# Kernel optimization log

Hardware: AMD Instinct MI355X
Metric: run time of the kernel (lower is better)

## Reference

```python
import jax, jax.numpy as jnp
import numpy as np

TOL = 5               # proximity_tolerance
PROX_REWARD = 2.0     # proximity_reward
FAR_PENALTY = 1.5     # far_penalty
CLASS_WEIGHTS = np.array([0.1, 5.0, 5.0], dtype=np.float32)


def setup_inputs() -> dict:
    key = jax.random.key(0)
    k1, k2 = jax.random.split(key)
    B, S, C = 512, 16384, 3
    logits = jax.random.normal(k1, (B, S, C), dtype=jnp.float32)
    labels = jax.random.randint(k2, (B, S), 0, 3)
    return {"logits": logits, "labels": labels}


def _window_any(mask_bool, tol):
    # True at position p iff mask is True anywhere in [p-tol, p+tol] (clipped at edges).
    pooled = jax.lax.reduce_window(
        mask_bool.astype(jnp.float32), 0.0, jax.lax.max,
        window_dimensions=(1, 2 * tol + 1), window_strides=(1, 1),
        padding=[(0, 0), (tol, tol)])
    return pooled > 0.5


def reference(logits, labels):
    B, S, C = logits.shape
    w = jnp.asarray(CLASS_WEIGHTS)

    valid = labels != -100                      # [B,S]
    labels_safe = jnp.where(valid, labels, 0)

    # Weighted cross-entropy, reduction='none' (weight applied per-element, ignore_index -> 0)
    logp = jax.nn.log_softmax(logits, axis=-1)  # [B,S,C]
    picked = jnp.take_along_axis(logp, labels_safe[..., None], axis=-1)[..., 0]
    base_loss = jnp.where(valid, -w[labels_safe] * picked, 0.0)  # [B,S]

    predictions = jnp.argmax(logits, axis=-1)   # [B,S] int
    pred_sw = predictions >= 1                  # predicted switch positions
    true_sw = labels >= 1                       # true switch positions (-100 < 1 so excluded)

    pred_near = _window_any(pred_sw, TOL)       # any predicted switch within +/-TOL
    true_near = _window_any(true_sw, TOL)       # any true switch within +/-TOL
    has_true = jnp.any(true_sw, axis=1, keepdims=True)  # far-penalty only applies if batch row has true switches

    reward_mask = (true_sw & pred_near).astype(jnp.float32)
    penalty_mask = (pred_sw & (~true_near) & has_true).astype(jnp.float32)
    additive = -PROX_REWARD * reward_mask + FAR_PENALTY * penalty_mask

    vm = valid.astype(jnp.float32)
    return ((base_loss + additive) * vm).sum() / vm.sum()
```

## Files before the change

### kernel.cpp

```cpp
#include <hip/hip_runtime.h>
#include <hip/hip_bf16.h>


#define TOL 5
#define BLOCK 256
#define CHUNK 1024

typedef unsigned long long u64;

__global__ __launch_bounds__(BLOCK) void k1_stream(
    const float* __restrict__ logits, const int* __restrict__ labels,
    u64* __restrict__ pmask, u64* __restrict__ tmask, u64* __restrict__ vmask,
    double* __restrict__ pbsum, int* __restrict__ pvcnt)
{
    __shared__ float lds_l[CHUNK * 3];
    __shared__ int   lds_lab[CHUNK];
    __shared__ float wb[BLOCK / 64];
    __shared__ int   wv[BLOCK / 64];

    const int tid = threadIdx.x;
    const long long chunk = blockIdx.x;

    const float4* gl4 = (const float4*)logits + chunk * (CHUNK * 3 / 4);
    float4* ll4 = (float4*)lds_l;
#pragma unroll
    for (int k = 0; k < 3; ++k) ll4[tid + k * BLOCK] = gl4[tid + k * BLOCK];
    const int4* gi4 = (const int4*)labels + chunk * (CHUNK / 4);
    ((int4*)lds_lab)[tid] = gi4[tid];
    __syncthreads();

    float bsum = 0.f;
    int   vcnt = 0;
    const int wave = tid >> 6;
    const u64 base_group = (u64)chunk * (CHUNK / 64);

#pragma unroll
    for (int q = 0; q < CHUNK / BLOCK; ++q) {
        const int pos = q * BLOCK + tid;
        const float l0 = lds_l[3 * pos + 0];
        const float l1 = lds_l[3 * pos + 1];
        const float l2 = lds_l[3 * pos + 2];
        const int lab = lds_lab[pos];

        const bool valid = (lab != -100);
        const int ls = valid ? lab : 0;

        const float mx = fmaxf(l0, fmaxf(l1, l2));
        const float se = __expf(l0 - mx) + __expf(l1 - mx) + __expf(l2 - mx);
        const float lse = mx + __logf(se);
        const float lpick = (ls == 0 ? l0 : (ls == 1 ? l1 : l2)) - lse;
        const float w = (ls == 0) ? 0.1f : 5.0f;
        bsum += valid ? (-w * lpick) : 0.f;
        vcnt += valid ? 1 : 0;

        const bool psw = fmaxf(l1, l2) > l0;
        const bool tsw = (lab >= 1);

        const u64 pm = __ballot(psw);
        const u64 tm = __ballot(tsw);
        const u64 vm = __ballot(valid);
        if ((tid & 63) == 0) {
            const u64 g = base_group + (u64)(q * (BLOCK / 64) + wave);
            pmask[g] = pm; tmask[g] = tm; vmask[g] = vm;
        }
    }

#pragma unroll
    for (int off = 32; off; off >>= 1) {
        bsum += __shfl_down(bsum, off);
        vcnt += __shfl_down(vcnt, off);
    }
    if ((tid & 63) == 0) { wb[wave] = bsum; wv[wave] = vcnt; }
    __syncthreads();
    if (tid == 0) {
        double s = 0.0; int c = 0;
#pragma unroll
        for (int i = 0; i < BLOCK / 64; ++i) { s += (double)wb[i]; c += wv[i]; }
        pbsum[chunk] = s;
        pvcnt[chunk] = c;
    }
}

__global__ __launch_bounds__(BLOCK) void k2_window(
    const u64* __restrict__ pmask, const u64* __restrict__ tmask,
    const u64* __restrict__ vmask, float* __restrict__ adj_row)
{
    const int row = blockIdx.x;
    const int t = threadIdx.x;
    const int GPR = BLOCK;
    const long long base = (long long)row * GPR + t;

    const u64 pm = pmask[base];
    const u64 tm = tmask[base];
    const u64 vm = vmask[base];
    const u64 pp = (t > 0)       ? pmask[base - 1] : 0ULL;
    const u64 pn = (t < GPR - 1) ? pmask[base + 1] : 0ULL;
    const u64 tp = (t > 0)       ? tmask[base - 1] : 0ULL;
    const u64 tn = (t < GPR - 1) ? tmask[base + 1] : 0ULL;

    u64 pnear = pm, tnear = tm;
#pragma unroll
    for (int k = 1; k <= TOL; ++k) {
        pnear |= (pm << k) | (pm >> k) | (pp >> (64 - k)) | (pn << (64 - k));
        tnear |= (tm << k) | (tm >> k) | (tp >> (64 - k)) | (tn << (64 - k));
    }

    int reward  = __popcll(tm & pnear);
    int penalty = __popcll(pm & ~tnear & vm);
    int ht = (tm != 0ULL) ? 1 : 0;

#pragma unroll
    for (int off = 32; off; off >>= 1) {
        reward  += __shfl_down(reward, off);
        penalty += __shfl_down(penalty, off);
        ht      |= __shfl_down(ht, off);
    }
    __shared__ int rs[BLOCK / 64], ps[BLOCK / 64], hs[BLOCK / 64];
    const int wave = t >> 6;
    if ((t & 63) == 0) { rs[wave] = reward; ps[wave] = penalty; hs[wave] = ht; }
    __syncthreads();
    if (t == 0) {
        int R = 0, P = 0, H = 0;
#pragma unroll
        for (int i = 0; i < BLOCK / 64; ++i) { R += rs[i]; P += ps[i]; H |= hs[i]; }
        adj_row[row] = -2.0f * (float)R + (H ? 1.5f * (float)P : 0.0f);
    }
}

__global__ __launch_bounds__(BLOCK) void k3_reduce(
    const double* __restrict__ pbsum, const int* __restrict__ pvcnt, int nblocks,
    const float* __restrict__ adj_row, int nrows,
    float* __restrict__ out)
{
    const int t = threadIdx.x;
    double s = 0.0, a = 0.0;
    long long c = 0;
    for (int i = t; i < nblocks; i += BLOCK) { s += pbsum[i]; c += (long long)pvcnt[i]; }
    for (int i = t; i < nrows; i += BLOCK) a += (double)adj_row[i];

#pragma unroll
    for (int off = 32; off; off >>= 1) {
        s += __shfl_down(s, off);
        a += __shfl_down(a, off);
        c += __shfl_down(c, off);
    }
    __shared__ double ss[BLOCK / 64], as[BLOCK / 64];
    __shared__ long long cs[BLOCK / 64];
    const int wave = t >> 6;
    if ((t & 63) == 0) { ss[wave] = s; as[wave] = a; cs[wave] = c; }
    __syncthreads();
    if (t == 0) {
        double S = 0.0, A = 0.0; long long C = 0;
#pragma unroll
        for (int i = 0; i < BLOCK / 64; ++i) { S += ss[i]; A += as[i]; C += cs[i]; }
        out[0] = (float)((S + A) / (double)C);
    }
}

extern "C" void kernel_launch(void* const* d_in, const int* in_sizes, int n_in,
                              void* d_out, int out_size, void* d_ws, size_t ws_size,
                              hipStream_t stream) {
    const float* logits = (const float*)d_in[0];
    const int*   labels = (const int*)d_in[1];
    float* out = (float*)d_out;

    const long long BS = in_sizes[1];
    const long long NGROUP = BS / 64;
    const int B = 512;
    const long long nchunk = BS / CHUNK;

    char* ws = (char*)d_ws;
    u64* pmask = (u64*)ws;
    u64* tmask = pmask + NGROUP;
    u64* vmask = tmask + NGROUP;
    double* pbsum = (double*)(vmask + NGROUP);
    int* pvcnt    = (int*)(pbsum + nchunk);
    float* adjrow = (float*)(pvcnt + nchunk);

    k1_stream<<<(dim3)(unsigned)nchunk, BLOCK, 0, stream>>>(
        logits, labels, pmask, tmask, vmask, pbsum, pvcnt);
    k2_window<<<B, BLOCK, 0, stream>>>(pmask, tmask, vmask, adjrow);
    k3_reduce<<<1, BLOCK, 0, stream>>>(pbsum, pvcnt, (int)nchunk, adjrow, B, out);
}
```

Measured before the change: 182.2 us.

## Read logits directly from global memory in a grid-stride persistent stream kernel

Removes the LDS staging of logits and labels in the first kernel, so each thread now loads its three logits with strided scalar global loads. The kernel also becomes grid-stride over a fixed grid of 2048 blocks instead of one block per chunk, which shrinks the per-block partial-sum arrays. The goal is to drop shared-memory traffic and the barrier and cut block-launch overhead, at the cost of less coalesced 12-byte-strided global loads in place of float4 vector loads.

After: 183.0 us. No clear change (+0.5%).

```diff
diff --git a/kernel.cpp b/kernel.cpp
--- a/kernel.cpp
+++ b/kernel.cpp
@@ -5,63 +5,52 @@
 #define TOL 5
 #define BLOCK 256
 #define CHUNK 1024
+#define GRID1 2048
 
 typedef unsigned long long u64;
 
-__global__ __launch_bounds__(BLOCK) void k1_stream(
+__global__ __launch_bounds__(BLOCK) void k1_direct(
     const float* __restrict__ logits, const int* __restrict__ labels,
     u64* __restrict__ pmask, u64* __restrict__ tmask, u64* __restrict__ vmask,
-    double* __restrict__ pbsum, int* __restrict__ pvcnt)
+    double* __restrict__ pbsum, int* __restrict__ pvcnt, long long nchunk)
 {
-    __shared__ float lds_l[CHUNK * 3];
-    __shared__ int   lds_lab[CHUNK];
-    __shared__ float wb[BLOCK / 64];
-    __shared__ int   wv[BLOCK / 64];
-
     const int tid = threadIdx.x;
-    const long long chunk = blockIdx.x;
-
-    const float4* gl4 = (const float4*)logits + chunk * (CHUNK * 3 / 4);
-    float4* ll4 = (float4*)lds_l;
-#pragma unroll
-    for (int k = 0; k < 3; ++k) ll4[tid + k * BLOCK] = gl4[tid + k * BLOCK];
-    const int4* gi4 = (const int4*)labels + chunk * (CHUNK / 4);
-    ((int4*)lds_lab)[tid] = gi4[tid];
-    __syncthreads();
+    const int wave = tid >> 6;
 
     float bsum = 0.f;
     int   vcnt = 0;
-    const int wave = tid >> 6;
-    const u64 base_group = (u64)chunk * (CHUNK / 64);
 
+    for (long long c = blockIdx.x; c < nchunk; c += GRID1) {
+        const long long base = c * CHUNK;
 #pragma unroll
-    for (int q = 0; q < CHUNK / BLOCK; ++q) {
-        const int pos = q * BLOCK + tid;
-        const float l0 = lds_l[3 * pos + 0];
-        const float l1 = lds_l[3 * pos + 1];
-        const float l2 = lds_l[3 * pos + 2];
-        const int lab = lds_lab[pos];
+        for (int q = 0; q < CHUNK / BLOCK; ++q) {
+            const long long p = base + q * BLOCK + tid;
+            const float l0 = logits[3 * p + 0];
+            const float l1 = logits[3 * p + 1];
+            const float l2 = logits[3 * p + 2];
+            const int lab = labels[p];
 
-        const bool valid = (lab != -100);
-        const int ls = valid ? lab : 0;
+            const bool valid = (lab != -100);
+            const int ls = valid ? lab : 0;
 
-        const float mx = fmaxf(l0, fmaxf(l1, l2));
-        const float se = __expf(l0 - mx) + __expf(l1 - mx) + __expf(l2 - mx);
-        const float lse = mx + __logf(se);
-        const float lpick = (ls == 0 ? l0 : (ls == 1 ? l1 : l2)) - lse;
-        const float w = (ls == 0) ? 0.1f : 5.0f;
-        bsum += valid ? (-w * lpick) : 0.f;
-        vcnt += valid ? 1 : 0;
+            const float mx = fmaxf(l0, fmaxf(l1, l2));
+            const float se = __expf(l0 - mx) + __expf(l1 - mx) + __expf(l2 - mx);
+            const float lse = mx + __logf(se);
+            const float lpick = (ls == 0 ? l0 : (ls == 1 ? l1 : l2)) - lse;
+            const float w = (ls == 0) ? 0.1f : 5.0f;
+            bsum += valid ? (-w * lpick) : 0.f;
+            vcnt += valid ? 1 : 0;
 
-        const bool psw = fmaxf(l1, l2) > l0;
-        const bool tsw = (lab >= 1);
+            const bool psw = fmaxf(l1, l2) > l0;
+            const bool tsw = (lab >= 1);
 
-        const u64 pm = __ballot(psw);
-        const u64 tm = __ballot(tsw);
-        const u64 vm = __ballot(valid);
-        if ((tid & 63) == 0) {
-            const u64 g = base_group + (u64)(q * (BLOCK / 64) + wave);
-            pmask[g] = pm; tmask[g] = tm; vmask[g] = vm;
+            const u64 pm = __ballot(psw);
+            const u64 tm = __ballot(tsw);
+            const u64 vm = __ballot(valid);
+            if ((tid & 63) == 0) {
+                const long long g = (base + q * BLOCK + wave * 64) >> 6;
+                pmask[g] = pm; tmask[g] = tm; vmask[g] = vm;
+            }
         }
     }
 
@@ -70,14 +59,16 @@
         bsum += __shfl_down(bsum, off);
         vcnt += __shfl_down(vcnt, off);
     }
+    __shared__ float wb[BLOCK / 64];
+    __shared__ int   wv[BLOCK / 64];
     if ((tid & 63) == 0) { wb[wave] = bsum; wv[wave] = vcnt; }
     __syncthreads();
     if (tid == 0) {
-        double s = 0.0; int c = 0;
+        double s = 0.0; int cc = 0;
 #pragma unroll
-        for (int i = 0; i < BLOCK / 64; ++i) { s += (double)wb[i]; c += wv[i]; }
-        pbsum[chunk] = s;
-        pvcnt[chunk] = c;
+        for (int i = 0; i < BLOCK / 64; ++i) { s += (double)wb[i]; cc += wv[i]; }
+        pbsum[blockIdx.x] = s;
+        pvcnt[blockIdx.x] = cc;
     }
 }
 
@@ -174,11 +165,11 @@
     u64* tmask = pmask + NGROUP;
     u64* vmask = tmask + NGROUP;
     double* pbsum = (double*)(vmask + NGROUP);
-    int* pvcnt    = (int*)(pbsum + nchunk);
-    float* adjrow = (float*)(pvcnt + nchunk);
+    int* pvcnt    = (int*)(pbsum + GRID1);
+    float* adjrow = (float*)(pvcnt + GRID1);
 
-    k1_stream<<<(dim3)(unsigned)nchunk, BLOCK, 0, stream>>>(
-        logits, labels, pmask, tmask, vmask, pbsum, pvcnt);
+    k1_direct<<<GRID1, BLOCK, 0, stream>>>(
+        logits, labels, pmask, tmask, vmask, pbsum, pvcnt, nchunk);
     k2_window<<<B, BLOCK, 0, stream>>>(pmask, tmask, vmask, adjrow);
-    k3_reduce<<<1, BLOCK, 0, stream>>>(pbsum, pvcnt, (int)nchunk, adjrow, B, out);
+    k3_reduce<<<1, BLOCK, 0, stream>>>(pbsum, pvcnt, GRID1, adjrow, B, out);
 }
```
